# Kernel optimization log

Measured on AMD Instinct MI355X. Metric: run time of the kernel, lower is better.

The kernel has to match this reference:

```python
import jax, jax.numpy as jnp
import numpy as np

N, E, C, H, G, NC = 100000, 1600000, 128, 128, 256, 10
NEG_SLOPE = 0.2


def setup_inputs() -> dict:
    key = jax.random.key(0)
    ks = jax.random.split(key, 12)
    return {
        "x": jax.random.normal(ks[0], (N, C), jnp.float32),
        "edge_index": jax.random.randint(ks[1], (2, E), 0, N),
        "edge_attr": jax.random.uniform(ks[2], (E,), jnp.float32),
        "batch": jnp.sort(jax.random.randint(ks[3], (N,), 0, G)),
        "num_graphs": G,
        "att": jax.random.normal(ks[4], (3, 2 * C), jnp.float32) * (6.0 / (1 + 2 * C)) ** 0.5,
        "W1": jax.random.normal(ks[5], (3, C, H), jnp.float32) * (1.0 / C) ** 0.5,
        "b1": jnp.zeros((3, H), jnp.float32),
        "W2": jax.random.normal(ks[6], (3, H, H), jnp.float32) * (1.0 / H) ** 0.5,
        "b2": jnp.zeros((3, H), jnp.float32),
        "fc1_w": jax.random.normal(ks[7], (6 * H, 2 * H), jnp.float32) * (1.0 / (6 * H)) ** 0.5,
        "fc1_b": jnp.zeros((2 * H,), jnp.float32),
        "fc2_w": jax.random.normal(ks[8], (2 * H, H), jnp.float32) * (1.0 / (2 * H)) ** 0.5,
        "fc2_b": jnp.zeros((H,), jnp.float32),
        "fc3_w": jax.random.normal(ks[9], (H, NC), jnp.float32) * (1.0 / H) ** 0.5,
        "fc3_b": jnp.zeros((NC,), jnp.float32),
    }


def segment_sparsemax(z, seg, num_segments):
    """Exact sparsemax within each segment (ragged), vectorized via lexsort."""
    n = z.shape[0]
    order = jnp.lexsort((-z, seg))          # by segment asc, value desc
    zs, ss = z[order], seg[order]
    counts = jax.ops.segment_sum(jnp.ones((n,), jnp.int32), seg, num_segments)
    starts = jnp.cumsum(counts) - counts    # exclusive prefix -> segment start
    pos = jnp.arange(n, dtype=jnp.int32) - starts[ss]   # 0-based rank in segment
    ecs = jnp.cumsum(zs)
    base = jnp.concatenate([jnp.zeros((1,), zs.dtype), ecs])[starts[ss]]
    segcum = ecs - base                     # inclusive within-segment cumsum
    cond = 1.0 + (pos + 1).astype(zs.dtype) * zs > segcum  # support prefix mask
    k = jax.ops.segment_sum(cond.astype(zs.dtype), ss, num_segments)
    sum_k = jax.ops.segment_sum(jnp.where(cond, zs, 0.0), ss, num_segments)
    tau = jnp.where(k > 0, (sum_k - 1.0) / jnp.maximum(k, 1.0), 0.0)
    return jnp.maximum(z - tau[seg], 0.0)


def gcn_conv(x, row, col, ew, W, b, n_nodes):
    """PyG GCNConv with edge weights + self-loops (fill value 1)."""
    h = x @ W                                            # [N, H]
    deg = jax.ops.segment_sum(ew, col, n_nodes) + 1.0    # self-loop weight 1
    dinv = jnp.where(deg > 0, jax.lax.rsqrt(deg), 0.0)
    norm = dinv[row] * ew * dinv[col]                    # per-edge norm
    out = jax.ops.segment_sum(norm[:, None] * h[row], col, n_nodes)
    out = out + h * (dinv * dinv)[:, None]               # self-loop contribution
    return out + b


def emodel_block(x, row, col, att_b, W1_b, b1_b, W2_b, b2_b, n_nodes):
    # Edgelayer: att * cat([x[row], x[col]]) summed -> leaky_relu -> sparsemax(row)
    c = x.shape[1]
    s1 = x @ att_b[:c]                                   # [N]
    s2 = x @ att_b[c:]
    w = s1[row] + s2[col]
    w = jnp.where(w >= 0, w, NEG_SLOPE * w)              # leaky_relu
    p = segment_sparsemax(w, row, n_nodes)               # zero weight == pruned edge
    h = jax.nn.relu(gcn_conv(x, row, col, p, W1_b, b1_b, n_nodes))
    h = jax.nn.relu(gcn_conv(h, row, col, p, W2_b, b2_b, n_nodes))
    return h


def global_pools(z, batch, num_graphs):
    cnt = jax.ops.segment_sum(jnp.ones((z.shape[0], 1), z.dtype), batch, num_graphs)
    mean = jax.ops.segment_sum(z, batch, num_graphs) / jnp.maximum(cnt, 1.0)
    mx = jax.ops.segment_max(z, batch, num_graphs)
    mx = jnp.where(jnp.isfinite(mx), mx, 0.0)            # guard empty graphs
    return mean, mx


def reference(x, edge_index, edge_attr, batch, num_graphs, att, W1, b1, W2, b2,
              fc1_w, fc1_b, fc2_w, fc2_b, fc3_w, fc3_b):
    n_nodes = x.shape[0]
    row, col = edge_index[0], edge_index[1]
    feats = []
    for i in range(3):  # three structurally identical blocks with distinct params
        z = emodel_block(x, row, col, att[i], W1[i], b1[i], W2[i], b2[i], n_nodes)
        mean, mx = global_pools(z, batch, num_graphs)
        feats += [mean, mx]
    h = jnp.concatenate(feats, axis=1)                   # [G, 6*H]
    h = jax.nn.relu(h @ fc1_w + fc1_b)
    h = jax.nn.relu(h @ fc2_w + fc2_b)
    return jax.nn.log_softmax(h @ fc3_w + fc3_b, axis=-1)
```

## Files before the change

### kernel.cpp

```cpp
#include <hip/hip_runtime.h>
#include <math.h>

constexpr int NN   = 100000;
constexpr int EE   = 1600000;
constexpr int CH   = 128;
constexpr int GG   = 256;
constexpr int NCLS = 10;
constexpr int SW   = 48;
constexpr int QW   = 24;

constexpr int NB   = (NN + 63) >> 6;
constexpr int BCAP = 1344;
constexpr int EPT  = 8;
constexpr int BINTB = 256;
constexpr int EPB  = BINTB * EPT;

typedef _Float16 half8  __attribute__((ext_vector_type(8)));
typedef _Float16 half4  __attribute__((ext_vector_type(4)));
typedef _Float16 half2v __attribute__((ext_vector_type(2)));
typedef float    float4v __attribute__((ext_vector_type(4)));

__global__ void bounds_kernel(const int* __restrict__ batch, int* __restrict__ gb,
                              int* __restrict__ bcur) {
    int t = blockIdx.x * blockDim.x + threadIdx.x;
    if (t < NB) bcur[t] = 0;
    if (t > GG) return;
    int lo = 0, hi = NN;
    while (lo < hi) {
        int mid = (lo + hi) >> 1;
        if (batch[mid] < t) lo = mid + 1; else hi = mid;
    }
    gb[t] = lo;
}

__global__ void wt16_kernel(const float* __restrict__ W1, const float* __restrict__ W2,
                            _Float16* __restrict__ wt) {
    int mat = blockIdx.x;
    const float* src = (mat < 3) ? (W1 + (size_t)mat * 16384)
                                 : (W2 + (size_t)(mat - 3) * 16384);
    _Float16* dst = wt + (size_t)mat * 16384;
    for (int i = threadIdx.x; i < 16384; i += 256) {
        int n = i >> 7, k = i & 127;
        dst[n * 128 + k] = (_Float16)src[k * 128 + n];
    }
}

__global__ void scores3_kernel(const float* __restrict__ x, const float* __restrict__ att,
                               float* __restrict__ s1, float* __restrict__ s2,
                               int* __restrict__ cur, _Float16* __restrict__ x16) {
    int wid  = threadIdx.x >> 6;
    int lane = threadIdx.x & 63;
    int grp  = lane >> 4;
    int l16  = lane & 15;
    int node = blockIdx.x * 16 + wid * 4 + grp;
    if (node >= NN) return;
    const float4v* xp = (const float4v*)(x + (size_t)node * CH);
    float4v xa = xp[l16];
    float4v xb = xp[16 + l16];
    half4 ha, hb;
#pragma unroll
    for (int j = 0; j < 4; ++j) { ha[j] = (_Float16)xa[j]; hb[j] = (_Float16)xb[j]; }
    ((half4*)x16)[(size_t)node * 32 + l16]      = ha;
    ((half4*)x16)[(size_t)node * 32 + 16 + l16] = hb;
#pragma unroll
    for (int i = 0; i < 3; ++i) {
        const float* a = att + i * 256;
        float p1 = 0.f, p2 = 0.f;
#pragma unroll
        for (int j = 0; j < 4; ++j) {
            p1 += xa[j] * a[l16 * 4 + j];
            p1 += xb[j] * a[64 + l16 * 4 + j];
            p2 += xa[j] * a[128 + l16 * 4 + j];
            p2 += xb[j] * a[192 + l16 * 4 + j];
        }
#pragma unroll
        for (int off = 8; off > 0; off >>= 1) {
            p1 += __shfl_xor(p1, off, 64);
            p2 += __shfl_xor(p2, off, 64);
        }
        if (l16 == 0) { s1[i * NN + node] = p1; s2[i * NN + node] = p2; }
    }
    if (l16 == 0) {
        cur[node]          = 0;
        cur[NN + node]     = 0;
        cur[2 * NN + node] = 0;
    }
}

__global__ __launch_bounds__(256) void bin_kernel(const int* __restrict__ ei,
                                                  int* __restrict__ bcur,
                                                  unsigned int* __restrict__ binned) {
    __shared__ int hist[NB];
    __shared__ int basearr[NB];
    int tid = threadIdx.x;
    for (int b = tid; b < NB; b += BINTB) hist[b] = 0;
    __syncthreads();
    int e0 = blockIdx.x * EPB;
    int r[EPT], c[EPT], off[EPT];
#pragma unroll
    for (int j = 0; j < EPT; ++j) {
        int e = e0 + j * BINTB + tid;
        if (e < EE) {
            r[j] = ei[e];
            c[j] = ei[EE + e];
            off[j] = atomicAdd(&hist[r[j] >> 6], 1);
        } else r[j] = -1;
    }
    __syncthreads();
    for (int b = tid; b < NB; b += BINTB) {
        int n = hist[b];
        basearr[b] = n ? atomicAdd(&bcur[b], n) : 0;
    }
    __syncthreads();
#pragma unroll
    for (int j = 0; j < EPT; ++j) {
        if (r[j] >= 0) {
            int b = r[j] >> 6;
            int pos = basearr[b] + off[j];
            if (pos < BCAP)
                binned[(size_t)b * BCAP + pos] = (unsigned)(r[j] & 63) | ((unsigned)c[j] << 6);
        }
    }
}

__global__ __launch_bounds__(512) void buildtau_kernel(const int* __restrict__ bcur,
                                                       const unsigned int* __restrict__ binned,
                                                       const float* __restrict__ s1,
                                                       const float* __restrict__ s2,
                                                       float* __restrict__ taubuf) {
    __shared__ int slot[64 * SW];
    __shared__ int cntl[64];
    __shared__ int listA[64], listB[64], listC[64];
    __shared__ int nA, nB, nC;
    int b   = blockIdx.x;
    int tid = threadIdx.x;
    if (tid < 64) cntl[tid] = 0;
    if (tid == 0) { nA = 0; nB = 0; nC = 0; }
    __syncthreads();
    int cnt = min(bcur[b], BCAP);
    for (int idx = tid; idx < cnt; idx += 512) {
        unsigned u = binned[(size_t)b * BCAP + idx];
        int rlo = u & 63;
        int p = atomicAdd(&cntl[rlo], 1);
        if (p < SW) slot[rlo * SW + p] = (int)(u >> 6);
    }
    __syncthreads();
    if (tid < 64) {
        int d = min(cntl[tid], SW);
        if (d > 0) {
            if (d <= 16)      listA[atomicAdd(&nA, 1)] = tid;
            else if (d <= 32) listB[atomicAdd(&nB, 1)] = tid;
            else              listC[atomicAdd(&nC, 1)] = tid;
        }
    }
    __syncthreads();
    int wid = tid >> 6, lane = tid & 63;
    const float NEGINF = __int_as_float(0xff800000);

    {
        int grp = lane >> 4, l16 = lane & 15;
        for (int ia = wid * 4; ia < nA; ia += 32) {
            int idx   = min(ia + grp, nA - 1);
            int myrlo = listA[idx];
            int mydeg = (ia + grp < nA) ? min(cntl[myrlo], SW) : 0;
            int vv    = (b << 6) + myrlo;
            int c = (l16 < mydeg) ? slot[myrlo * SW + l16] : 0;
            float z[3];
#pragma unroll
            for (int i = 0; i < 3; ++i) {
                z[i] = NEGINF;
                if (l16 < mydeg) {
                    float w = s1[i * NN + vv] + s2[i * NN + c];
                    z[i] = (w >= 0.f) ? w : 0.2f * w;
                }
            }
#pragma unroll
            for (int k = 2; k <= 16; k <<= 1) {
#pragma unroll
                for (int j = k >> 1; j > 0; j >>= 1) {
                    bool keepMax = ((l16 & j) == 0) == ((l16 & k) == 0);
#pragma unroll
                    for (int i = 0; i < 3; ++i) {
                        float other = __shfl_xor(z[i], j, 64);
                        z[i] = keepMax ? fmaxf(z[i], other) : fminf(z[i], other);
                    }
                }
            }
            float cs[3];
#pragma unroll
            for (int i = 0; i < 3; ++i) cs[i] = z[i];
#pragma unroll
            for (int off = 1; off < 16; off <<= 1) {
#pragma unroll
                for (int i = 0; i < 3; ++i) {
                    float t = __shfl_up(cs[i], off, 64);
                    if (l16 >= off) cs[i] += t;
                }
            }
#pragma unroll
            for (int i = 0; i < 3; ++i) {
                bool cond = (l16 < mydeg) && (1.f + (float)(l16 + 1) * z[i] > cs[i]);
                unsigned long long m = __ballot(cond);
                int myk = __popcll((m >> (grp * 16)) & 0xFFFFull);
                float sumk = __shfl(cs[i], grp * 16 + max(myk, 1) - 1, 64);
                if (l16 == 0 && mydeg > 0)
                    taubuf[i * NN + vv] = (sumk - 1.f) / (float)max(myk, 1);
            }
        }
    }

    {
        int half = lane >> 5, l32 = lane & 31;
        for (int ib = wid * 2; ib < nB; ib += 16) {
            int idx   = min(ib + half, nB - 1);
            int myrlo = listB[idx];
            int mydeg = (ib + half < nB) ? min(cntl[myrlo], SW) : 0;
            int vv    = (b << 6) + myrlo;
            int c = (l32 < mydeg) ? slot[myrlo * SW + l32] : 0;
            float z[3];
#pragma unroll
            for (int i = 0; i < 3; ++i) {
                z[i] = NEGINF;
                if (l32 < mydeg) {
                    float w = s1[i * NN + vv] + s2[i * NN + c];
                    z[i] = (w >= 0.f) ? w : 0.2f * w;
                }
            }
#pragma unroll
            for (int k = 2; k <= 32; k <<= 1) {
#pragma unroll
                for (int j = k >> 1; j > 0; j >>= 1) {
                    bool keepMax = ((l32 & j) == 0) == ((l32 & k) == 0);
#pragma unroll
                    for (int i = 0; i < 3; ++i) {
                        float other = __shfl_xor(z[i], j, 64);
                        z[i] = keepMax ? fmaxf(z[i], other) : fminf(z[i], other);
                    }
                }
            }
            float cs[3];
#pragma unroll
            for (int i = 0; i < 3; ++i) cs[i] = z[i];
#pragma unroll
            for (int off = 1; off < 32; off <<= 1) {
#pragma unroll
                for (int i = 0; i < 3; ++i) {
                    float t = __shfl_up(cs[i], off, 64);
                    if (l32 >= off) cs[i] += t;
                }
            }
#pragma unroll
            for (int i = 0; i < 3; ++i) {
                bool cond = (l32 < mydeg) && (1.f + (float)(l32 + 1) * z[i] > cs[i]);
                unsigned long long m = __ballot(cond);
                int myk = half ? __popcll(m >> 32) : __popcll(m & 0xFFFFFFFFull);
                float sumk = __shfl(cs[i], half * 32 + max(myk, 1) - 1, 64);
                if (l32 == 0 && mydeg > 0)
                    taubuf[i * NN + vv] = (sumk - 1.f) / (float)max(myk, 1);
            }
        }
    }

    for (int ic = wid; ic < nC; ic += 8) {
        int rlo = listC[ic];
        int deg = min(cntl[rlo], SW);
        int v   = (b << 6) + rlo;
        int c = (lane < deg) ? slot[rlo * SW + lane] : 0;
#pragma unroll
        for (int i = 0; i < 3; ++i) {
            float z = NEGINF;
            if (lane < deg) {
                float w = s1[i * NN + v] + s2[i * NN + c];
                z = (w >= 0.f) ? w : 0.2f * w;
            }
#pragma unroll
            for (int k = 2; k <= 64; k <<= 1) {
#pragma unroll
                for (int j = k >> 1; j > 0; j >>= 1) {
                    float other = __shfl_xor(z, j, 64);
                    bool keepMax = ((lane & j) == 0) == ((lane & k) == 0);
                    z = keepMax ? fmaxf(z, other) : fminf(z, other);
                }
            }
            float cs = z;
#pragma unroll
            for (int off = 1; off < 64; off <<= 1) {
                float t = __shfl_up(cs, off, 64);
                if (lane >= off) cs += t;
            }
            bool cond = (lane < deg) && (1.f + (float)(lane + 1) * z > cs);
            unsigned long long mask = __ballot(cond);
            int k = __popcll(mask);
            float sumk = __shfl(cs, k - 1, 64);
            if (lane == 0) taubuf[i * NN + v] = (sumk - 1.f) / (float)k;
        }
    }
}

__global__ void compact_kernel(const int* __restrict__ ei, const float* __restrict__ s1,
                               const float* __restrict__ s2, const float* __restrict__ taubuf,
                               int* __restrict__ qcnt, int2* __restrict__ qslot) {
    int e = blockIdx.x * blockDim.x + threadIdx.x;
    if (e >= EE) return;
    int r = ei[e], c = ei[EE + e];
    float w = s1[r] + s2[c];
    w = (w >= 0.f) ? w : 0.2f * w;
    float p = w - taubuf[r];
    if (p > 0.f) {
        int pos = atomicAdd(&qcnt[c], 1);
        if (pos < QW) qslot[c * QW + pos] = make_int2(r, __float_as_int(p));
    }
}

__global__ void degq_kernel(const int* __restrict__ qcnt, const int2* __restrict__ qslot,
                            float* __restrict__ dinv) {
    int v = blockIdx.x * blockDim.x + threadIdx.x;
    if (v >= NN) return;
    int cnt = min(qcnt[v], QW);
    double d = 1.0;
    int base = v * QW;
    for (int t = 0; t < cnt; ++t) d += (double)__int_as_float(qslot[base + t].y);
    dinv[v] = rsqrtf((float)d);
}

__global__ __launch_bounds__(256) void gemm16_kernel(const _Float16* __restrict__ A,
                                                     const _Float16* __restrict__ WT,
                                                     _Float16* __restrict__ Cout, int M) {
    int lane = threadIdx.x & 63;
    int wid  = threadIdx.x >> 6;
    int l15  = lane & 15;
    int quad = lane >> 4;
    int rowbase = blockIdx.x * 64 + wid * 16;
    int arow = rowbase + l15;

    float4v acc[8];
#pragma unroll
    for (int n = 0; n < 8; ++n) acc[n] = (float4v){0.f, 0.f, 0.f, 0.f};

#pragma unroll
    for (int kc = 0; kc < 4; ++kc) {
        half8 a = {};
        if (arow < M) a = *(const half8*)(A + (size_t)arow * CH + kc * 32 + quad * 8);
#pragma unroll
        for (int n = 0; n < 8; ++n) {
            half8 b = *(const half8*)(WT + (size_t)(n * 16 + l15) * CH + kc * 32 + quad * 8);
            acc[n] = __builtin_amdgcn_mfma_f32_16x16x32_f16(a, b, acc[n], 0, 0, 0);
        }
    }
#pragma unroll
    for (int n = 0; n < 8; ++n) {
#pragma unroll
        for (int r = 0; r < 4; ++r) {
            int row = rowbase + quad * 4 + r;
            if (row < M) Cout[(size_t)row * CH + n * 16 + l15] = (_Float16)acc[n][r];
        }
    }
}

__global__ void agg_kernel(const _Float16* __restrict__ hin,
                           const int* __restrict__ qcnt, const int2* __restrict__ qslot,
                           const float* __restrict__ dinv, const float* __restrict__ bias,
                           _Float16* __restrict__ out) {
    int wid  = threadIdx.x >> 6;
    int lane = threadIdx.x & 63;
    int grp  = lane >> 4;
    int l16  = lane & 15;
    int v = blockIdx.x * 16 + wid * 4 + grp;
    if (v >= NN) return;
    const half8* hin8 = (const half8*)hin;
    int cnt  = min(qcnt[v], QW);
    int base = v * QW;
    float dv = dinv[v];
    double acc[8];
#pragma unroll
    for (int j = 0; j < 8; ++j) acc[j] = 0.0;
    for (int t = 0; t < cnt; ++t) {
        int2 ep = qslot[base + t];
        int r = ep.x;
        float g = __int_as_float(ep.y) * dinv[r];
        half8 hr = hin8[(size_t)r * 16 + l16];
#pragma unroll
        for (int j = 0; j < 8; ++j)
            acc[j] += (double)g * (double)(float)hr[j];
    }
    half8 hv = hin8[(size_t)v * 16 + l16];
    const float* bp = bias + l16 * 8;
    half8 o;
#pragma unroll
    for (int j = 0; j < 8; ++j) {
        float oo = fmaxf(dv * (float)acc[j] + dv * dv * (float)hv[j] + bp[j], 0.f);
        o[j] = (_Float16)oo;
    }
    ((half8*)out)[(size_t)v * 16 + l16] = o;
}

__global__ void pool_kernel(const _Float16* __restrict__ z, const int* __restrict__ gb,
                            float* __restrict__ feats, int blk) {
    int g = blockIdx.x;
    int f = threadIdx.x;
    int s = gb[g], e = gb[g + 1];
    float sum = 0.f, mx = 0.f;
    const _Float16* zp = z + (size_t)s * CH + f;
    int n = s;
    for (; n + 16 <= e; n += 16) {
        float v[16];
#pragma unroll
        for (int j = 0; j < 16; ++j) v[j] = (float)zp[(size_t)j * CH];
#pragma unroll
        for (int j = 0; j < 16; ++j) {
            sum += v[j];
            mx = fmaxf(mx, v[j]);
        }
        zp += (size_t)16 * CH;
    }
    for (; n < e; ++n) {
        float v = (float)*zp;
        sum += v;
        mx = fmaxf(mx, v);
        zp += CH;
    }
    int cnt = e - s;
    feats[g * 768 + blk * 256 + f]       = sum / (float)max(cnt, 1);
    feats[g * 768 + blk * 256 + 128 + f] = mx;
}

__global__ void fc1_kernel(const float* __restrict__ feats, const float* __restrict__ w,
                           const float* __restrict__ b, float* __restrict__ t1) {
    __shared__ float lf[768];
    int g = blockIdx.x, j = threadIdx.x;
    for (int i = j; i < 768; i += 256) lf[i] = feats[g * 768 + i];
    __syncthreads();
    float acc = b[j];
    for (int k = 0; k < 768; ++k) acc += lf[k] * w[k * 256 + j];
    t1[g * 256 + j] = fmaxf(acc, 0.f);
}

__global__ void fc23_kernel(const float* __restrict__ t1,
                            const float* __restrict__ w2, const float* __restrict__ b2,
                            const float* __restrict__ w3, const float* __restrict__ b3,
                            float* __restrict__ out) {
    __shared__ float lt[256];
    __shared__ float lh[128];
    __shared__ float lg[NCLS];
    int g = blockIdx.x, j = threadIdx.x;
    lt[j]       = t1[g * 256 + j];
    lt[j + 128] = t1[g * 256 + 128 + j];
    __syncthreads();
    float acc = b2[j];
    for (int k = 0; k < 256; ++k) acc += lt[k] * w2[k * 128 + j];
    lh[j] = fmaxf(acc, 0.f);
    __syncthreads();
    if (j < NCLS) {
        float a = b3[j];
        for (int k = 0; k < 128; ++k) a += lh[k] * w3[k * NCLS + j];
        lg[j] = a;
    }
    __syncthreads();
    if (j == 0) {
        float mxv = lg[0];
        for (int i = 1; i < NCLS; ++i) mxv = fmaxf(mxv, lg[i]);
        float se = 0.f;
        for (int i = 0; i < NCLS; ++i) se += expf(lg[i] - mxv);
        float lse = logf(se) + mxv;
        for (int i = 0; i < NCLS; ++i) out[g * NCLS + i] = lg[i] - lse;
    }
}

extern "C" void kernel_launch(void* const* d_in, const int* in_sizes, int n_in,
                              void* d_out, int out_size, void* d_ws, size_t ws_size,
                              hipStream_t stream) {
    const float* x     = (const float*)d_in[0];
    const int*   ei    = (const int*)  d_in[1];
    const int*   batch = (const int*)  d_in[3];
    const float* att   = (const float*)d_in[5];
    const float* W1    = (const float*)d_in[6];
    const float* b1    = (const float*)d_in[7];
    const float* W2    = (const float*)d_in[8];
    const float* b2    = (const float*)d_in[9];
    const float* fc1w  = (const float*)d_in[10];
    const float* fc1b  = (const float*)d_in[11];
    const float* fc2w  = (const float*)d_in[12];
    const float* fc2b  = (const float*)d_in[13];
    const float* fc3w  = (const float*)d_in[14];
    const float* fc3b  = (const float*)d_in[15];
    float* out = (float*)d_out;

    char* p = (char*)d_ws;
    auto carve = [&](size_t bytes) -> void* {
        void* r = (void*)p;
        p += (bytes + 255) & ~(size_t)255;
        return r;
    };
    int* cur  = (int*)carve((size_t)3 * NN * 4);
    int* qcnt = cur;
    void* adj = carve((size_t)NN * QW * 8);
    unsigned int* binned = (unsigned int*)adj;
    int2*         qslot  = (int2*)adj;
    int* gb   = (int*)carve((size_t)(GG + 1) * 4);
    int* bcur = (int*)carve((size_t)NB * 4);
    float* s1     = (float*)carve((size_t)3 * NN * 4);
    float* s2     = (float*)carve((size_t)3 * NN * 4);
    float* taubuf = (float*)carve((size_t)3 * NN * 4);
    float* dinv   = (float*)carve((size_t)NN * 4);
    _Float16* wt16 = (_Float16*)carve((size_t)6 * 16384 * 2);
    _Float16* x16  = (_Float16*)carve((size_t)NN * CH * 2);
    _Float16* bufA = (_Float16*)carve((size_t)NN * CH * 2);
    _Float16* bufB = (_Float16*)carve((size_t)NN * CH * 2);
    float* feats  = (float*)carve((size_t)GG * 768 * 4);
    float* t1     = (float*)carve((size_t)GG * 256 * 4);

    const int TB = 256;
    dim3 egrid((EE + TB - 1) / TB);
    dim3 ngrid((NN + TB - 1) / TB);
    dim3 sgrid((NN + 15) / 16);
    dim3 ggrid((NN + 63) / 64);
    dim3 bingrid((EE + EPB - 1) / EPB);
    dim3 bgrid((NB + TB - 1) / TB);

    scores3_kernel<<<sgrid, 256, 0, stream>>>(x, att, s1, s2, cur, x16);
    bounds_kernel<<<bgrid, TB, 0, stream>>>(batch, gb, bcur);
    bin_kernel<<<bingrid, BINTB, 0, stream>>>(ei, bcur, binned);
    wt16_kernel<<<6, 256, 0, stream>>>(W1, W2, wt16);
    buildtau_kernel<<<NB, 512, 0, stream>>>(bcur, binned, s1, s2, taubuf);

    for (int i = 0; i < 3; ++i) {
        const float* s1_i  = s1 + (size_t)i * NN;
        const float* s2_i  = s2 + (size_t)i * NN;
        const float* tau_i = taubuf + (size_t)i * NN;
        int*         qc_i  = qcnt + (size_t)i * NN;
        const _Float16* WT1_i = wt16 + (size_t)i * 16384;
        const _Float16* WT2_i = wt16 + (size_t)(3 + i) * 16384;
        const float* b1_i  = b1 + i * CH;
        const float* b2_i  = b2 + i * CH;

        compact_kernel<<<egrid, TB, 0, stream>>>(ei, s1_i, s2_i, tau_i, qc_i, qslot);
        degq_kernel<<<ngrid, TB, 0, stream>>>(qc_i, qslot, dinv);

        gemm16_kernel<<<ggrid, 256, 0, stream>>>(x16, WT1_i, bufA, NN);
        agg_kernel<<<sgrid, 256, 0, stream>>>(bufA, qc_i, qslot, dinv, b1_i, bufB);
        gemm16_kernel<<<ggrid, 256, 0, stream>>>(bufB, WT2_i, bufA, NN);
        agg_kernel<<<sgrid, 256, 0, stream>>>(bufA, qc_i, qslot, dinv, b2_i, bufB);

        pool_kernel<<<GG, 128, 0, stream>>>(bufB, gb, feats, i);
    }

    fc1_kernel<<<GG, 256, 0, stream>>>(feats, fc1w, fc1b, t1);
    fc23_kernel<<<GG, 128, 0, stream>>>(t1, fc2w, fc2b, fc3w, fc3b, out);
}
```

Baseline: 835.9 us.

## Split edge binning into coarse 1024-node pass and fine 64-node pass

Replaces the single-pass edge binning into 64-node bins with a two-level scheme. The first pass bins edges into 1024-node coarse buckets using a small shared histogram and few global atomics. A second kernel then splits each coarse bucket into 16 fine bins using shared-memory atomics. The aim is to cut the per-block shared histogram initialisation and the global atomic traffic over about 1563 bins, at the cost of one extra launch and an extra pass over the edges. It also changes the order of edges within each bin.

```diff
diff --git a/kernel.cpp b/kernel.cpp
--- a/kernel.cpp
+++ b/kernel.cpp
@@ -9,8 +9,11 @@
 constexpr int SW   = 48;
 constexpr int QW   = 24;
 
-constexpr int NB   = (NN + 63) >> 6;
-constexpr int BCAP = 1344;
+constexpr int NB    = (NN + 63) >> 6;
+constexpr int BCAP  = 1344;
+constexpr int NCB   = (NN + 1023) >> 10;
+constexpr int CBCAP = 18432;
+constexpr int FPC   = 16;
 constexpr int EPT  = 8;
 constexpr int BINTB = 256;
 constexpr int EPB  = BINTB * EPT;
@@ -21,9 +24,9 @@
 typedef float    float4v __attribute__((ext_vector_type(4)));
 
 __global__ void bounds_kernel(const int* __restrict__ batch, int* __restrict__ gb,
-                              int* __restrict__ bcur) {
+                              int* __restrict__ ccur) {
     int t = blockIdx.x * blockDim.x + threadIdx.x;
-    if (t < NB) bcur[t] = 0;
+    if (t < NCB) ccur[t] = 0;
     if (t > GG) return;
     int lo = 0, hi = NN;
     while (lo < hi) {
@@ -87,13 +90,13 @@
     }
 }
 
-__global__ __launch_bounds__(256) void bin_kernel(const int* __restrict__ ei,
-                                                  int* __restrict__ bcur,
-                                                  unsigned int* __restrict__ binned) {
-    __shared__ int hist[NB];
-    __shared__ int basearr[NB];
+__global__ __launch_bounds__(256) void binc_kernel(const int* __restrict__ ei,
+                                                   int* __restrict__ ccur,
+                                                   unsigned int* __restrict__ coarse) {
+    __shared__ int hist[NCB];
+    __shared__ int basearr[NCB];
     int tid = threadIdx.x;
-    for (int b = tid; b < NB; b += BINTB) hist[b] = 0;
+    if (tid < NCB) hist[tid] = 0;
     __syncthreads();
     int e0 = blockIdx.x * EPB;
     int r[EPT], c[EPT], off[EPT];
@@ -103,23 +106,48 @@
         if (e < EE) {
             r[j] = ei[e];
             c[j] = ei[EE + e];
-            off[j] = atomicAdd(&hist[r[j] >> 6], 1);
+            off[j] = atomicAdd(&hist[r[j] >> 10], 1);
         } else r[j] = -1;
     }
     __syncthreads();
-    for (int b = tid; b < NB; b += BINTB) {
-        int n = hist[b];
-        basearr[b] = n ? atomicAdd(&bcur[b], n) : 0;
+    if (tid < NCB) {
+        int n = hist[tid];
+        basearr[tid] = n ? atomicAdd(&ccur[tid], n) : 0;
     }
     __syncthreads();
 #pragma unroll
     for (int j = 0; j < EPT; ++j) {
         if (r[j] >= 0) {
-            int b = r[j] >> 6;
+            int b = r[j] >> 10;
             int pos = basearr[b] + off[j];
-            if (pos < BCAP)
-                binned[(size_t)b * BCAP + pos] = (unsigned)(r[j] & 63) | ((unsigned)c[j] << 6);
-        }
+            if (pos < CBCAP)
+                coarse[(size_t)b * CBCAP + pos] = (unsigned)(r[j] & 1023) | ((unsigned)c[j] << 10);
+        }
+    }
+}
+
+__global__ __launch_bounds__(512) void binf_kernel(const int* __restrict__ ccur,
+                                                   const unsigned int* __restrict__ coarse,
+                                                   int* __restrict__ bcur,
+                                                   unsigned int* __restrict__ binned) {
+    __shared__ int cnt2[FPC];
+    int cb = blockIdx.x, tid = threadIdx.x;
+    if (tid < FPC) cnt2[tid] = 0;
+    __syncthreads();
+    int cnt = min(ccur[cb], CBCAP);
+    for (int idx = tid; idx < cnt; idx += 512) {
+        unsigned u = coarse[(size_t)cb * CBCAP + idx];
+        int fl = (u & 1023) >> 6;
+        int pos = atomicAdd(&cnt2[fl], 1);
+        if (pos < BCAP) {
+            int fg = cb * FPC + fl;
+            binned[(size_t)fg * BCAP + pos] = (u & 63) | ((u >> 10) << 6);
+        }
+    }
+    __syncthreads();
+    if (tid < FPC) {
+        int fg = cb * FPC + tid;
+        if (fg < NB) bcur[fg] = cnt2[tid];
     }
 }
 
@@ -495,9 +523,11 @@
     int* qcnt = cur;
     void* adj = carve((size_t)NN * QW * 8);
     unsigned int* binned = (unsigned int*)adj;
+    unsigned int* coarse = binned + (size_t)NB * BCAP;
     int2*         qslot  = (int2*)adj;
     int* gb   = (int*)carve((size_t)(GG + 1) * 4);
     int* bcur = (int*)carve((size_t)NB * 4);
+    int* ccur = (int*)carve((size_t)NCB * 4);
     float* s1     = (float*)carve((size_t)3 * NN * 4);
     float* s2     = (float*)carve((size_t)3 * NN * 4);
     float* taubuf = (float*)carve((size_t)3 * NN * 4);
@@ -515,12 +545,12 @@
     dim3 sgrid((NN + 15) / 16);
     dim3 ggrid((NN + 63) / 64);
     dim3 bingrid((EE + EPB - 1) / EPB);
-    dim3 bgrid((NB + TB - 1) / TB);
 
     scores3_kernel<<<sgrid, 256, 0, stream>>>(x, att, s1, s2, cur, x16);
-    bounds_kernel<<<bgrid, TB, 0, stream>>>(batch, gb, bcur);
-    bin_kernel<<<bingrid, BINTB, 0, stream>>>(ei, bcur, binned);
+    bounds_kernel<<<2, 256, 0, stream>>>(batch, gb, ccur);
+    binc_kernel<<<bingrid, BINTB, 0, stream>>>(ei, ccur, coarse);
     wt16_kernel<<<6, 256, 0, stream>>>(W1, W2, wt16);
+    binf_kernel<<<NCB, 512, 0, stream>>>(ccur, coarse, bcur, binned);
     buildtau_kernel<<<NB, 512, 0, stream>>>(bcur, binned, s1, s2, taubuf);
 
     for (int i = 0; i < 3; ++i) {
```

New measurement: 834.3 us. About the same (-0.2%).
